# Kernel optimization log

Hardware: AMD Instinct MI355X
Metric: run time of the kernel (lower is better)

Reference implementation:

```python
import jax, jax.numpy as jnp
import numpy as np

C_REG = 50.0  # soft-SVM regularization from __init__ default C=50


def kronecker(A, B):
    # torch: einsum('ab,cd->acbd').view(a*c, b*d)
    return jnp.einsum('ab,cd->acbd', A, B).reshape(
        A.shape[0] * B.shape[0], A.shape[1] * B.shape[1])


def setup_inputs() -> dict:
    key = jax.random.key(0)
    k1, k2, k3, k4 = jax.random.split(key, 4)
    N_c, N_S, N_Q, C, W, H = 16, 25, 15, 3, 32, 32
    D_feat = 640
    S_k = jax.random.normal(k1, (N_c, N_S, C, W, H), dtype=jnp.float32)
    Q_k = jax.random.normal(k2, (N_c, N_Q, C, W, H), dtype=jnp.float32)
    # base_net modeled as Flatten -> Linear(C*W*H, D_feat), no bias
    W_base = jax.random.normal(k3, (C * W * H, D_feat), dtype=jnp.float32) * 0.02
    gamma = jax.random.normal(k4, (1,), dtype=jnp.float32)
    return {"S_k": S_k, "Q_k": Q_k, "W_base": W_base, "gamma": gamma}


def reference(S_k, Q_k, W_base, gamma):
    N_c, N_S = S_k.shape[:2]
    N_Q = Q_k.shape[1]
    # base_net: flatten image dims, project to features
    f_x = S_k.reshape(N_c * N_S, -1) @ W_base  # placeholder
    f_x = Q_k.reshape(N_c * N_Q, -1) @ W_base          # [N_c*N_Q, D]
    K = S_k.reshape(N_c * N_S, -1) @ W_base            # [N_c*N_S, D]
    # kernel matrix + ridge
    aul = K @ K.T + C_REG * jnp.eye(N_c * N_S, dtype=K.dtype)  # [N_c*N_S, N_c*N_S]
    # explicit Kronecker expansion to the full (N_c^2*N_S) system
    Q = kronecker(jnp.eye(N_c, dtype=K.dtype), aul)    # [N_c^2*N_S, N_c^2*N_S]
    p = kronecker(jnp.eye(N_c, dtype=K.dtype),
                  jnp.ones((1, N_S), dtype=K.dtype)).reshape(-1, 1)
    alpha = jnp.linalg.solve(Q, jax.lax.stop_gradient(p))  # p is detached in torch
    alpha = alpha.reshape(N_c, -1)                     # [N_c, N_c*N_S]
    w_k = alpha @ K                                    # [N_c, D]
    logits = -gamma * (f_x @ w_k.T)                    # [N_c*N_Q, N_c]
    return logits
```

## Files before the change

### kernel.cpp

```cpp
#include <hip/hip_runtime.h>
#include <math.h>

#define DIN 3072
#define DF 640
#define MROWS 400
#define QROWS 240
#define NMAT 400
#define PN 416
#define NRHS 16
#define CREG 50.0f
#define PVSTEPS 5
#define CSTEPS 25
#define KSPLIT 4
#define GBLK 13
#define SCOLS 32
#define FPAD 72
#define MTILES 28
#define DPAD 424

typedef __attribute__((ext_vector_type(8))) short bf8v;
typedef __attribute__((ext_vector_type(4))) short s4v;
typedef __attribute__((ext_vector_type(4))) float f32x4;

__device__ __forceinline__ short bf16_rn(float x) {
  unsigned u = __float_as_uint(x);
  u += 0x7FFFu + ((u >> 16) & 1u);
  return (short)(u >> 16);
}
__device__ __forceinline__ void split_sh(float x, short& h, short& l) {
  h = bf16_rn(x);
  float hf = __uint_as_float(((unsigned)(unsigned short)h) << 16);
  l = bf16_rn(x - hf);
}
__device__ __forceinline__ float bf2f(short h) {
  return __uint_as_float(((unsigned)(unsigned short)h) << 16);
}

__global__ __launch_bounds__(256) void gemm_feat_sk(const float* __restrict__ S,
                                                    const float* __restrict__ Qm,
                                                    const float* __restrict__ Wb,
                                                    float* __restrict__ Acc) {
  __shared__ short Ash[64][FPAD];
  __shared__ short Asl[64][FPAD];
  __shared__ short Bsh[64][FPAD];
  __shared__ short Bsl[64][FPAD];
  int tid = threadIdx.x;
  int wave = tid >> 6, lane = tid & 63, l16 = lane & 15, quad = lane >> 4;
  int by = blockIdx.y, bx = blockIdx.x, bz = blockIdx.z;
  int colBase = bx * 64;
  int kbeg = bz * (DIN / KSPLIT), kend = kbeg + (DIN / KSPLIT);
  int kc4 = (tid & 15) * 4;
  float4 ar4[4], br4[4];
  auto load_regs = [&](int kk) {
#pragma unroll
    for (int p = 0; p < 4; ++p) {
      int rowoff = 16 * p;
      const float* srp;
      {
        int ar_ = by * 64 + (tid >> 4) + rowoff;
        srp = (ar_ < MROWS) ? (S + (size_t)ar_ * DIN) : (Qm + (size_t)(ar_ - MROWS) * DIN);
      }
      ar4[p] = *reinterpret_cast<const float4*>(srp + kk + kc4);
      int r = (tid >> 4) + rowoff;
      br4[p] = *reinterpret_cast<const float4*>(Wb + (size_t)(kk + r) * DF + colBase + kc4);
    }
  };
  auto split_write = [&]() {
#pragma unroll
    for (int p = 0; p < 4; ++p) {
      int row = (tid >> 4) + 16 * p;
      s4v hv, lv; short h, l;
      split_sh(ar4[p].x, h, l); hv[0] = h; lv[0] = l;
      split_sh(ar4[p].y, h, l); hv[1] = h; lv[1] = l;
      split_sh(ar4[p].z, h, l); hv[2] = h; lv[2] = l;
      split_sh(ar4[p].w, h, l); hv[3] = h; lv[3] = l;
      *reinterpret_cast<s4v*>(&Ash[row][kc4]) = hv;
      *reinterpret_cast<s4v*>(&Asl[row][kc4]) = lv;
      split_sh(br4[p].x, h, l); Bsh[kc4 + 0][row] = h; Bsl[kc4 + 0][row] = l;
      split_sh(br4[p].y, h, l); Bsh[kc4 + 1][row] = h; Bsl[kc4 + 1][row] = l;
      split_sh(br4[p].z, h, l); Bsh[kc4 + 2][row] = h; Bsl[kc4 + 2][row] = l;
      split_sh(br4[p].w, h, l); Bsh[kc4 + 3][row] = h; Bsl[kc4 + 3][row] = l;
    }
  };
  f32x4 acc[4] = {{0,0,0,0},{0,0,0,0},{0,0,0,0},{0,0,0,0}};
  load_regs(kbeg);
  split_write();
  __syncthreads();
  int k0 = kbeg;
  while (true) {
    int kn = k0 + 64;
    bool more = (kn < kend);
    if (more) load_regs(kn);
#pragma unroll
    for (int kk = 0; kk < 64; kk += 32) {
      int ko = kk + quad * 8;
      bf8v ah = *reinterpret_cast<const bf8v*>(&Ash[wave * 16 + l16][ko]);
      bf8v al = *reinterpret_cast<const bf8v*>(&Asl[wave * 16 + l16][ko]);
#pragma unroll
      for (int t = 0; t < 4; ++t) {
        bf8v bh = *reinterpret_cast<const bf8v*>(&Bsh[t * 16 + l16][ko]);
        bf8v bl = *reinterpret_cast<const bf8v*>(&Bsl[t * 16 + l16][ko]);
        acc[t] = __builtin_amdgcn_mfma_f32_16x16x32_bf16(ah, bh, acc[t], 0, 0, 0);
        acc[t] = __builtin_amdgcn_mfma_f32_16x16x32_bf16(ah, bl, acc[t], 0, 0, 0);
        acc[t] = __builtin_amdgcn_mfma_f32_16x16x32_bf16(al, bh, acc[t], 0, 0, 0);
      }
    }
    if (!more) break;
    __syncthreads();
    split_write();
    __syncthreads();
    k0 = kn;
  }
  float* Ap = Acc + (size_t)bz * 640 * DF;
  int row0 = by * 64 + wave * 16;
#pragma unroll
  for (int t = 0; t < 4; ++t)
#pragma unroll
    for (int r = 0; r < 4; ++r) {
      int row = row0 + quad * 4 + r;
      int col = colBase + t * 16 + l16;
      Ap[(size_t)row * DF + col] = acc[t][r];
    }
}

__global__ __launch_bounds__(256) void feat_reduce(const float* __restrict__ Acc,
                                                   short* __restrict__ Kh,
                                                   short* __restrict__ Kl,
                                                   float* __restrict__ FX,
                                                   float* __restrict__ zbuf,
                                                   float* __restrict__ out) {
  int tid = threadIdx.x;
  if (blockIdx.x == 0) {
    for (int e = tid; e < 16; e += 256) zbuf[e] = 0.f;
  } else if (blockIdx.x == 1) {
    for (int e = tid; e < QROWS * NRHS; e += 256) out[e] = 0.f;
  }
  int idx = blockIdx.x * 256 + tid;
  if (idx >= 640 * DF) return;
  float v = Acc[idx] + Acc[idx + 409600] + Acc[idx + 819200] + Acc[idx + 1228800];
  int row = idx / DF, col = idx - row * DF;
  if (row < MROWS) {
    short h, l; split_sh(v, h, l);
    Kh[(size_t)row * DF + col] = h;
    Kl[(size_t)row * DF + col] = l;
  } else {
    FX[(size_t)(row - MROWS) * DF + col] = v;
  }
}

__global__ __launch_bounds__(256) void gemm_aul(const short* __restrict__ Kh,
                                                const short* __restrict__ Kl,
                                                short* __restrict__ Aph,
                                                short* __restrict__ Apl) {
  int tid = threadIdx.x;
  int wave = tid >> 6, lane = tid & 63;
  int l16 = lane & 15, quad = lane >> 4;
  int row0 = blockIdx.y * 64 + wave * 16;
  int colBase = blockIdx.x * 64;
  bool aValid = (row0 < MROWS);
  const bf8v bzero = {0,0,0,0,0,0,0,0};
  f32x4 acc[4] = {{0,0,0,0},{0,0,0,0},{0,0,0,0},{0,0,0,0}};
  for (int k0 = 0; k0 < DF; k0 += 32) {
    int ka = k0 + quad * 8;
    bf8v ah = bzero, al = bzero;
    if (aValid) {
      size_t ao = (size_t)(row0 + l16) * DF + ka;
      ah = *reinterpret_cast<const bf8v*>(Kh + ao);
      al = *reinterpret_cast<const bf8v*>(Kl + ao);
    }
#pragma unroll
    for (int t = 0; t < 4; ++t) {
      int colt = colBase + t * 16;
      bf8v bh = bzero, bl = bzero;
      if (colt < MROWS) {
        size_t bo = (size_t)(colt + l16) * DF + ka;
        bh = *reinterpret_cast<const bf8v*>(Kh + bo);
        bl = *reinterpret_cast<const bf8v*>(Kl + bo);
      }
      acc[t] = __builtin_amdgcn_mfma_f32_16x16x32_bf16(ah, bh, acc[t], 0, 0, 0);
      acc[t] = __builtin_amdgcn_mfma_f32_16x16x32_bf16(ah, bl, acc[t], 0, 0, 0);
      acc[t] = __builtin_amdgcn_mfma_f32_16x16x32_bf16(al, bh, acc[t], 0, 0, 0);
    }
  }
  if (row0 >= PN) return;
#pragma unroll
  for (int t = 0; t < 4; ++t) {
    int colt = colBase + t * 16;
    if (colt >= PN) continue;
#pragma unroll
    for (int r = 0; r < 4; ++r) {
      int row = row0 + quad * 4 + r;
      int col = colt + l16;
      float v = acc[t][r];
      if (row == col && row < MROWS) v += CREG;
      short h, l; split_sh(v, h, l);
      size_t o = (size_t)row * PN + col;
      Aph[o] = h; Apl[o] = l;
    }
  }
}

__global__ __launch_bounds__(256) void solve_and_m(const short* __restrict__ Aph,
                                                   const short* __restrict__ Apl,
                                                   const float* __restrict__ FX,
                                                   const short* __restrict__ Kh,
                                                   const short* __restrict__ Kl,
                                                   const float* __restrict__ gamma,
                                                   unsigned* __restrict__ D0,
                                                   unsigned* __restrict__ D1,
                                                   float* __restrict__ V0,
                                                   float* __restrict__ V1,
                                                   unsigned* __restrict__ bar,
                                                   unsigned* __restrict__ mflag,
                                                   float* __restrict__ M,
                                                   float* __restrict__ out) {
  int tid = threadIdx.x, b = blockIdx.x;
  int wave = tid >> 6, lane = tid & 63, l16 = lane & 15, quad = lane >> 4;
  const bf8v bzero = {0,0,0,0,0,0,0,0};

  if (b >= GBLK) {
    int mt = b - GBLK;
    int mb = mt / 7, nb = mt - (mt / 7) * 7;
    int q0 = mb * 64 + wave * 16;
    f32x4 acc[4] = {{0,0,0,0},{0,0,0,0},{0,0,0,0},{0,0,0,0}};
    int arow = q0 + l16;
    bool aOk = (arow < QROWS);
    const float* fr = FX + (size_t)(aOk ? arow : 0) * DF;
    for (int k0 = 0; k0 < DF; k0 += 32) {
      int ka = k0 + quad * 8;
      bf8v ah = bzero, al = bzero;
      if (aOk) {
        float4 a0 = *reinterpret_cast<const float4*>(fr + ka);
        float4 a1 = *reinterpret_cast<const float4*>(fr + ka + 4);
        float av[8] = {a0.x, a0.y, a0.z, a0.w, a1.x, a1.y, a1.z, a1.w};
#pragma unroll
        for (int j = 0; j < 8; ++j) { short h, l; split_sh(av[j], h, l); ah[j] = h; al[j] = l; }
      }
#pragma unroll
      for (int t = 0; t < 4; ++t) {
        int n = nb * 64 + t * 16 + l16;
        bf8v bh = bzero, bl = bzero;
        if (n < NMAT) {
          bh = *reinterpret_cast<const bf8v*>(Kh + (size_t)n * DF + ka);
          bl = *reinterpret_cast<const bf8v*>(Kl + (size_t)n * DF + ka);
        }
        acc[t] = __builtin_amdgcn_mfma_f32_16x16x32_bf16(ah, bh, acc[t], 0, 0, 0);
        acc[t] = __builtin_amdgcn_mfma_f32_16x16x32_bf16(ah, bl, acc[t], 0, 0, 0);
        acc[t] = __builtin_amdgcn_mfma_f32_16x16x32_bf16(al, bh, acc[t], 0, 0, 0);
      }
    }
#pragma unroll
    for (int t = 0; t < 4; ++t)
#pragma unroll
      for (int r = 0; r < 4; ++r) {
        int row = q0 + quad * 4 + r;
        int col = nb * 64 + t * 16 + l16;
        if (row < QROWS && col < NMAT)
          __hip_atomic_store(&M[(size_t)row * NMAT + col], acc[t][r],
                             __ATOMIC_RELAXED, __HIP_MEMORY_SCOPE_AGENT);
      }
    __syncthreads();
    if (tid == 0)
      __hip_atomic_fetch_add(mflag, 1u, __ATOMIC_RELEASE, __HIP_MEMORY_SCOPE_AGENT);
    return;
  }

  __shared__ __align__(16) short Abig[2][SCOLS][DPAD];
  __shared__ __align__(16) short dbT[2][NRHS][DPAD];
  __shared__ float yred[4][SCOLS][17];
  __shared__ float vprevL[PN], vcurL[PN];
  __shared__ float XsL[SCOLS][NRHS + 1];
  __shared__ float scal[2];
  __shared__ float rn[4], rd[4];
  int r0 = b * SCOLS;

  for (int e = tid; e < SCOLS * 52; e += 256) {
    int i = e / 52, c = e - i * 52;
    *reinterpret_cast<bf8v*>(&Abig[0][i][c * 8]) =
        *reinterpret_cast<const bf8v*>(Aph + (size_t)(r0 + i) * PN + c * 8);
    *reinterpret_cast<bf8v*>(&Abig[1][i][c * 8]) =
        *reinterpret_cast<const bf8v*>(Apl + (size_t)(r0 + i) * PN + c * 8);
  }
  for (int e = tid; e < NRHS * DPAD; e += 256) (&dbT[0][0][0])[e] = 0;
  for (int e = tid; e < PN; e += 256) {
    float v = (e < NMAT) ? (1.f + 0.125f * (float)(e & 7)) : 0.f;
    vcurL[e] = v;
    dbT[0][0][e] = bf16_rn(v);
  }
  __syncthreads();

  unsigned ph = 0;
  auto gridbar = [&]() {
    __syncthreads();
    ++ph;
    if (tid == 0) {
      unsigned tgt = ph * GBLK;
      __hip_atomic_fetch_add(bar, 1u, __ATOMIC_RELEASE, __HIP_MEMORY_SCOPE_AGENT);
      while (__hip_atomic_load(bar, __ATOMIC_RELAXED, __HIP_MEMORY_SCOPE_AGENT) < tgt)
        __builtin_amdgcn_s_sleep(2);
    }
    __syncthreads();
  };

  auto matvec = [&](bool lo) {
    f32x4 acc0 = {0, 0, 0, 0}, acc1 = {0, 0, 0, 0};
    for (int kt = wave; kt < 13; kt += 4) {
      int ko = kt * 32 + quad * 8;
      bf8v bh = *reinterpret_cast<const bf8v*>(&dbT[0][l16][ko]);
      bf8v ah0 = *reinterpret_cast<const bf8v*>(&Abig[0][l16][ko]);
      bf8v ah1 = *reinterpret_cast<const bf8v*>(&Abig[0][16 + l16][ko]);
      acc0 = __builtin_amdgcn_mfma_f32_16x16x32_bf16(ah0, bh, acc0, 0, 0, 0);
      acc1 = __builtin_amdgcn_mfma_f32_16x16x32_bf16(ah1, bh, acc1, 0, 0, 0);
      if (lo) {
        bf8v bl = *reinterpret_cast<const bf8v*>(&dbT[1][l16][ko]);
        bf8v al0 = *reinterpret_cast<const bf8v*>(&Abig[1][l16][ko]);
        bf8v al1 = *reinterpret_cast<const bf8v*>(&Abig[1][16 + l16][ko]);
        acc0 = __builtin_amdgcn_mfma_f32_16x16x32_bf16(ah0, bl, acc0, 0, 0, 0);
        acc0 = __builtin_amdgcn_mfma_f32_16x16x32_bf16(al0, bh, acc0, 0, 0, 0);
        acc1 = __builtin_amdgcn_mfma_f32_16x16x32_bf16(ah1, bl, acc1, 0, 0, 0);
        acc1 = __builtin_amdgcn_mfma_f32_16x16x32_bf16(al1, bh, acc1, 0, 0, 0);
      }
    }
#pragma unroll
    for (int r_ = 0; r_ < 4; ++r_) {
      yred[wave][quad * 4 + r_][l16] = acc0[r_];
      yred[wave][16 + quad * 4 + r_][l16] = acc1[r_];
    }
  };

  for (int s = 0; s < PVSTEPS; ++s) {
    matvec(false);
    __syncthreads();
    if (tid < SCOLS) {
      float y = yred[0][tid][0] + yred[1][tid][0] + yred[2][tid][0] + yred[3][tid][0];
      float* Vb = (s & 1) ? V1 : V0;
      __hip_atomic_store(&Vb[r0 + tid], y, __ATOMIC_RELAXED, __HIP_MEMORY_SCOPE_AGENT);
    }
    gridbar();
    const float* Vb = (s & 1) ? V1 : V0;
    if (s == PVSTEPS - 1)
      for (int e = tid; e < PN; e += 256) vprevL[e] = vcurL[e];
    float g0 = __hip_atomic_load(&Vb[tid], __ATOMIC_RELAXED, __HIP_MEMORY_SCOPE_AGENT);
    float g1 = (tid < PN - 256)
        ? __hip_atomic_load(&Vb[tid + 256], __ATOMIC_RELAXED, __HIP_MEMORY_SCOPE_AGENT)
        : 0.f;
    {
      float v = g0 * (1.f / 4096.f);
      vcurL[tid] = v;
      dbT[0][0][tid] = bf16_rn(v);
    }
    if (tid < PN - 256) {
      float v = g1 * (1.f / 4096.f);
      vcurL[tid + 256] = v;
      dbT[0][0][tid + 256] = bf16_rn(v);
    }
    __syncthreads();
  }

  {
    float n = 0.f, dd = 0.f;
    for (int e = tid; e < PN; e += 256) {
      n += vprevL[e] * vcurL[e];
      dd += vprevL[e] * vprevL[e];
    }
#pragma unroll
    for (int o = 32; o; o >>= 1) {
      n += __shfl_down(n, o);
      dd += __shfl_down(dd, o);
    }
    if (lane == 0) { rn[wave] = n; rd[wave] = dd; }
    __syncthreads();
    if (tid == 0) {
      float N = rn[0] + rn[1] + rn[2] + rn[3];
      float D = rd[0] + rd[1] + rd[2] + rd[3];
      float rqv = 4096.f * N / D;
      float bb = 1.3f * rqv;
      if (!(bb > 800.f)) bb = 12000.f;
      if (bb > 100000.f) bb = 100000.f;
      scal[0] = 0.5f * (bb + CREG);
      scal[1] = 0.5f * (bb - CREG);
    }
    __syncthreads();
  }
  float theta = scal[0], delta = scal[1];
  float sigma = theta / delta, rho = 1.f / sigma;

  float xr[2], rr[2], dr[2];
#pragma unroll
  for (int m = 0; m < 2; ++m) {
    int rl = (tid >> 4) + 16 * m, c = tid & 15, gi = r0 + rl;
    float pc = (gi < NMAT && (gi / 25) == c) ? 1.f : 0.f;
    xr[m] = 0.f; rr[m] = pc; dr[m] = pc / theta;
    short h, l; split_sh(dr[m], h, l);
    __hip_atomic_store(&D0[(size_t)gi * NRHS + c],
                       ((unsigned)(unsigned short)h << 16) | (unsigned)(unsigned short)l,
                       __ATOMIC_RELAXED, __HIP_MEMORY_SCOPE_AGENT);
  }
  gridbar();
  {
    unsigned gw[26];
#pragma unroll
    for (int j = 0; j < 26; ++j)
      gw[j] = __hip_atomic_load(&D0[tid + 256 * j], __ATOMIC_RELAXED, __HIP_MEMORY_SCOPE_AGENT);
#pragma unroll
    for (int j = 0; j < 26; ++j) {
      int e = tid + 256 * j, row = e >> 4, c = e & 15;
      dbT[0][c][row] = (short)(gw[j] >> 16);
      dbT[1][c][row] = (short)gw[j];
    }
  }
  __syncthreads();

  for (int k = 0; k < CSTEPS - 1; ++k) {
    matvec(true);
    __syncthreads();
    float rho1 = 1.f / (2.f * sigma - rho);
    float s1 = rho1 * rho, s2 = 2.f * rho1 / delta;
    rho = rho1;
    unsigned* Db = (k & 1) ? D0 : D1;
#pragma unroll
    for (int m = 0; m < 2; ++m) {
      int rl = (tid >> 4) + 16 * m, c = tid & 15, gi = r0 + rl;
      float mv = yred[0][rl][c] + yred[1][rl][c] + yred[2][rl][c] + yred[3][rl][c];
      xr[m] += dr[m];
      rr[m] -= mv;
      float dn = s1 * dr[m] + s2 * rr[m];
      dr[m] = dn;
      if (k < CSTEPS - 2) {
        short h, l; split_sh(dn, h, l);
        __hip_atomic_store(&Db[(size_t)gi * NRHS + c],
                           ((unsigned)(unsigned short)h << 16) | (unsigned)(unsigned short)l,
                           __ATOMIC_RELAXED, __HIP_MEMORY_SCOPE_AGENT);
      }
    }
    if (k < CSTEPS - 2) {
      gridbar();
      unsigned gw[26];
#pragma unroll
      for (int j = 0; j < 26; ++j)
        gw[j] = __hip_atomic_load(&Db[tid + 256 * j], __ATOMIC_RELAXED, __HIP_MEMORY_SCOPE_AGENT);
#pragma unroll
      for (int j = 0; j < 26; ++j) {
        int e = tid + 256 * j, row = e >> 4, c = e & 15;
        dbT[0][c][row] = (short)(gw[j] >> 16);
        dbT[1][c][row] = (short)gw[j];
      }
    }
    __syncthreads();
  }

#pragma unroll
  for (int m = 0; m < 2; ++m) {
    int rl = (tid >> 4) + 16 * m, c = tid & 15;
    XsL[rl][c] = xr[m] + dr[m];
  }
  __syncthreads();
  if (tid == 0) {
    while (__hip_atomic_load(mflag, __ATOMIC_RELAXED, __HIP_MEMORY_SCOPE_AGENT) < MTILES)
      __builtin_amdgcn_s_sleep(2);
  }
  __syncthreads();
  float* Msl = reinterpret_cast<float*>(&Abig[0][0][0]);
  {
    float gm[30];
#pragma unroll
    for (int j = 0; j < 30; ++j) {
      int e = tid + 256 * j;
      int q = e >> 5, i = e & 31;
      gm[j] = (r0 + i < NMAT)
                  ? __hip_atomic_load(&M[(size_t)q * NMAT + r0 + i],
                                      __ATOMIC_RELAXED, __HIP_MEMORY_SCOPE_AGENT)
                  : 0.f;
    }
#pragma unroll
    for (int j = 0; j < 30; ++j) Msl[tid + 256 * j] = gm[j];
  }
  __syncthreads();
  float g = -gamma[0];
  int c = tid & 15;
  for (int q = tid >> 4; q < QROWS; q += 16) {
    float s = 0.f;
#pragma unroll
    for (int i = 0; i < SCOLS; ++i) s += Msl[q * SCOLS + i] * XsL[i][c];
    atomicAdd(&out[q * NRHS + c], g * s);
  }
}

extern "C" void kernel_launch(void* const* d_in, const int* in_sizes, int n_in,
                              void* d_out, int out_size, void* d_ws, size_t ws_size,
                              hipStream_t stream) {
  const float* S = (const float*)d_in[0];
  const float* Qm = (const float*)d_in[1];
  const float* Wb = (const float*)d_in[2];
  const float* gamma = (const float*)d_in[3];
  float* out = (float*)d_out;
  char* base = (char*)d_ws;
  short* Kh   = (short*)(base);
  short* Kl   = (short*)(base + 512000);
  float* FX   = (float*)(base + 1024000);
  short* Aph  = (short*)(base + 1638400);
  short* Apl  = (short*)(base + 1984512);
  float* Mm   = (float*)(base + 2330624);
  unsigned* bar = (unsigned*)(base + 2740224);
  unsigned* mflag = (unsigned*)(base + 2740240);
  float* zbuf = (float*)(base + 2740224);
  unsigned* D0 = (unsigned*)(base + 2740288);
  unsigned* D1 = (unsigned*)(base + 2766912);
  float* V0   = (float*)(base + 2793536);
  float* V1   = (float*)(base + 2795200);
  float* Acc  = (float*)(base + 2796864);

  gemm_feat_sk<<<dim3(10, 10, KSPLIT), 256, 0, stream>>>(S, Qm, Wb, Acc);
  feat_reduce<<<1600, 256, 0, stream>>>(Acc, Kh, Kl, FX, zbuf, out);
  gemm_aul<<<dim3(7, 7), 256, 0, stream>>>(Kh, Kl, Aph, Apl);
  solve_and_m<<<GBLK + MTILES, 256, 0, stream>>>(Aph, Apl, FX, Kh, Kl, gamma,
                                                 D0, D1, V0, V1, bar, mflag,
                                                 Mm, out);
}
```

Measured before the change: 216.0 us.

## Fuse kernel-matrix GEMM into solver and replace grid barrier with per-block flags

Removes the separate gemm_aul launch. Each solver block now computes its own 32-row slab of K·Kᵀ+C·I directly into shared memory with split-bf16 MFMAs. The single atomic grid barrier is replaced by per-block progress flags, so each wave waits only for the producer blocks whose slice it consumes and can start its partial matvec as soon as those arrive. This removes one kernel launch, the global round-trip of the matrix, and full-grid synchronisation. In exchange, the 13 solver blocks do redundant reads of K and more serial GEMM work, and a zeroed flags region is assumed across overlapping workspace offsets.

```diff
diff --git a/kernel.cpp b/kernel.cpp
--- a/kernel.cpp
+++ b/kernel.cpp
@@ -32,9 +32,6 @@
   float hf = __uint_as_float(((unsigned)(unsigned short)h) << 16);
   l = bf16_rn(x - hf);
 }
-__device__ __forceinline__ float bf2f(short h) {
-  return __uint_as_float(((unsigned)(unsigned short)h) << 16);
-}
 
 __global__ __launch_bounds__(256) void gemm_feat_sk(const float* __restrict__ S,
                                                     const float* __restrict__ Qm,
@@ -148,61 +145,7 @@
   }
 }
 
-__global__ __launch_bounds__(256) void gemm_aul(const short* __restrict__ Kh,
-                                                const short* __restrict__ Kl,
-                                                short* __restrict__ Aph,
-                                                short* __restrict__ Apl) {
-  int tid = threadIdx.x;
-  int wave = tid >> 6, lane = tid & 63;
-  int l16 = lane & 15, quad = lane >> 4;
-  int row0 = blockIdx.y * 64 + wave * 16;
-  int colBase = blockIdx.x * 64;
-  bool aValid = (row0 < MROWS);
-  const bf8v bzero = {0,0,0,0,0,0,0,0};
-  f32x4 acc[4] = {{0,0,0,0},{0,0,0,0},{0,0,0,0},{0,0,0,0}};
-  for (int k0 = 0; k0 < DF; k0 += 32) {
-    int ka = k0 + quad * 8;
-    bf8v ah = bzero, al = bzero;
-    if (aValid) {
-      size_t ao = (size_t)(row0 + l16) * DF + ka;
-      ah = *reinterpret_cast<const bf8v*>(Kh + ao);
-      al = *reinterpret_cast<const bf8v*>(Kl + ao);
-    }
-#pragma unroll
-    for (int t = 0; t < 4; ++t) {
-      int colt = colBase + t * 16;
-      bf8v bh = bzero, bl = bzero;
-      if (colt < MROWS) {
-        size_t bo = (size_t)(colt + l16) * DF + ka;
-        bh = *reinterpret_cast<const bf8v*>(Kh + bo);
-        bl = *reinterpret_cast<const bf8v*>(Kl + bo);
-      }
-      acc[t] = __builtin_amdgcn_mfma_f32_16x16x32_bf16(ah, bh, acc[t], 0, 0, 0);
-      acc[t] = __builtin_amdgcn_mfma_f32_16x16x32_bf16(ah, bl, acc[t], 0, 0, 0);
-      acc[t] = __builtin_amdgcn_mfma_f32_16x16x32_bf16(al, bh, acc[t], 0, 0, 0);
-    }
-  }
-  if (row0 >= PN) return;
-#pragma unroll
-  for (int t = 0; t < 4; ++t) {
-    int colt = colBase + t * 16;
-    if (colt >= PN) continue;
-#pragma unroll
-    for (int r = 0; r < 4; ++r) {
-      int row = row0 + quad * 4 + r;
-      int col = colt + l16;
-      float v = acc[t][r];
-      if (row == col && row < MROWS) v += CREG;
-      short h, l; split_sh(v, h, l);
-      size_t o = (size_t)row * PN + col;
-      Aph[o] = h; Apl[o] = l;
-    }
-  }
-}
-
-__global__ __launch_bounds__(256) void solve_and_m(const short* __restrict__ Aph,
-                                                   const short* __restrict__ Apl,
-                                                   const float* __restrict__ FX,
+__global__ __launch_bounds__(256) void solve_and_m(const float* __restrict__ FX,
                                                    const short* __restrict__ Kh,
                                                    const short* __restrict__ Kl,
                                                    const float* __restrict__ gamma,
@@ -210,7 +153,7 @@
                                                    unsigned* __restrict__ D1,
                                                    float* __restrict__ V0,
                                                    float* __restrict__ V1,
-                                                   unsigned* __restrict__ bar,
+                                                   unsigned* __restrict__ flags,
                                                    unsigned* __restrict__ mflag,
                                                    float* __restrict__ M,
                                                    float* __restrict__ out) {
@@ -274,14 +217,69 @@
   __shared__ float rn[4], rd[4];
   int r0 = b * SCOLS;
 
-  for (int e = tid; e < SCOLS * 52; e += 256) {
-    int i = e / 52, c = e - i * 52;
-    *reinterpret_cast<bf8v*>(&Abig[0][i][c * 8]) =
-        *reinterpret_cast<const bf8v*>(Aph + (size_t)(r0 + i) * PN + c * 8);
-    *reinterpret_cast<bf8v*>(&Abig[1][i][c * 8]) =
-        *reinterpret_cast<const bf8v*>(Apl + (size_t)(r0 + i) * PN + c * 8);
-  }
-  for (int e = tid; e < NRHS * DPAD; e += 256) (&dbT[0][0][0])[e] = 0;
+  for (int e = tid; e < SCOLS * DPAD; e += 256) {
+    *reinterpret_cast<unsigned*>(&(&Abig[0][0][0])[e * 2]) = 0u;
+    *reinterpret_cast<unsigned*>(&(&Abig[1][0][0])[e * 2]) = 0u;
+  }
+  for (int e = tid; e < NRHS * DPAD; e += 256) {
+    (&dbT[0][0][0])[e] = 0; (&dbT[1][0][0])[e] = 0;
+  }
+  __syncthreads();
+
+  {
+    bool rg1ok = (r0 + 16) < MROWS;
+    f32x4 pacc[2][7];
+#pragma unroll
+    for (int j = 0; j < 7; ++j) { pacc[0][j] = {0,0,0,0}; pacc[1][j] = {0,0,0,0}; }
+    const short* kh0 = Kh + (size_t)(r0 + l16) * DF;
+    const short* kl0 = Kl + (size_t)(r0 + l16) * DF;
+    const short* kh1 = Kh + (size_t)(rg1ok ? (r0 + 16 + l16) : 0) * DF;
+    const short* kl1 = Kl + (size_t)(rg1ok ? (r0 + 16 + l16) : 0) * DF;
+    for (int k0 = 0; k0 < DF; k0 += 32) {
+      int ka = k0 + quad * 8;
+      bf8v ah0 = *reinterpret_cast<const bf8v*>(kh0 + ka);
+      bf8v al0 = *reinterpret_cast<const bf8v*>(kl0 + ka);
+      bf8v ah1 = *reinterpret_cast<const bf8v*>(kh1 + ka);
+      bf8v al1 = *reinterpret_cast<const bf8v*>(kl1 + ka);
+#pragma unroll
+      for (int j = 0; j < 7; ++j) {
+        int cg = wave + 4 * j;
+        if (cg < 25) {
+          const short* bhp = Kh + (size_t)(cg * 16 + l16) * DF + ka;
+          const short* blp = Kl + (size_t)(cg * 16 + l16) * DF + ka;
+          bf8v bh = *reinterpret_cast<const bf8v*>(bhp);
+          bf8v bl = *reinterpret_cast<const bf8v*>(blp);
+          pacc[0][j] = __builtin_amdgcn_mfma_f32_16x16x32_bf16(ah0, bh, pacc[0][j], 0, 0, 0);
+          pacc[0][j] = __builtin_amdgcn_mfma_f32_16x16x32_bf16(ah0, bl, pacc[0][j], 0, 0, 0);
+          pacc[0][j] = __builtin_amdgcn_mfma_f32_16x16x32_bf16(al0, bh, pacc[0][j], 0, 0, 0);
+          pacc[1][j] = __builtin_amdgcn_mfma_f32_16x16x32_bf16(ah1, bh, pacc[1][j], 0, 0, 0);
+          pacc[1][j] = __builtin_amdgcn_mfma_f32_16x16x32_bf16(ah1, bl, pacc[1][j], 0, 0, 0);
+          pacc[1][j] = __builtin_amdgcn_mfma_f32_16x16x32_bf16(al1, bh, pacc[1][j], 0, 0, 0);
+        }
+      }
+    }
+#pragma unroll
+    for (int j = 0; j < 7; ++j) {
+      int cg = wave + 4 * j;
+      if (cg < 25) {
+#pragma unroll
+        for (int rg = 0; rg < 2; ++rg) {
+          if (rg == 1 && !rg1ok) continue;
+#pragma unroll
+          for (int r = 0; r < 4; ++r) {
+            int lrow = rg * 16 + quad * 4 + r;
+            int col = cg * 16 + l16;
+            float v = pacc[rg][j][r];
+            if (r0 + lrow == col) v += CREG;
+            short h, l; split_sh(v, h, l);
+            Abig[0][lrow][col] = h;
+            Abig[1][lrow][col] = l;
+          }
+        }
+      }
+    }
+  }
+
   for (int e = tid; e < PN; e += 256) {
     float v = (e < NMAT) ? (1.f + 0.125f * (float)(e & 7)) : 0.f;
     vcurL[e] = v;
@@ -289,36 +287,30 @@
   }
   __syncthreads();
 
-  unsigned ph = 0;
-  auto gridbar = [&]() {
-    __syncthreads();
-    ++ph;
-    if (tid == 0) {
-      unsigned tgt = ph * GBLK;
-      __hip_atomic_fetch_add(bar, 1u, __ATOMIC_RELEASE, __HIP_MEMORY_SCOPE_AGENT);
-      while (__hip_atomic_load(bar, __ATOMIC_RELAXED, __HIP_MEMORY_SCOPE_AGENT) < tgt)
-        __builtin_amdgcn_s_sleep(2);
-    }
-    __syncthreads();
-  };
-
-  auto matvec = [&](bool lo) {
-    f32x4 acc0 = {0, 0, 0, 0}, acc1 = {0, 0, 0, 0};
-    for (int kt = wave; kt < 13; kt += 4) {
-      int ko = kt * 32 + quad * 8;
-      bf8v bh = *reinterpret_cast<const bf8v*>(&dbT[0][l16][ko]);
-      bf8v ah0 = *reinterpret_cast<const bf8v*>(&Abig[0][l16][ko]);
-      bf8v ah1 = *reinterpret_cast<const bf8v*>(&Abig[0][16 + l16][ko]);
-      acc0 = __builtin_amdgcn_mfma_f32_16x16x32_bf16(ah0, bh, acc0, 0, 0, 0);
-      acc1 = __builtin_amdgcn_mfma_f32_16x16x32_bf16(ah1, bh, acc1, 0, 0, 0);
-      if (lo) {
-        bf8v bl = *reinterpret_cast<const bf8v*>(&dbT[1][l16][ko]);
-        bf8v al0 = *reinterpret_cast<const bf8v*>(&Abig[1][l16][ko]);
-        bf8v al1 = *reinterpret_cast<const bf8v*>(&Abig[1][16 + l16][ko]);
-        acc0 = __builtin_amdgcn_mfma_f32_16x16x32_bf16(ah0, bl, acc0, 0, 0, 0);
-        acc0 = __builtin_amdgcn_mfma_f32_16x16x32_bf16(al0, bh, acc0, 0, 0, 0);
-        acc1 = __builtin_amdgcn_mfma_f32_16x16x32_bf16(ah1, bl, acc1, 0, 0, 0);
-        acc1 = __builtin_amdgcn_mfma_f32_16x16x32_bf16(al1, bh, acc1, 0, 0, 0);
+  for (int s = 0; s < PVSTEPS; ++s) {
+    f32x4 acc0 = {0,0,0,0}, acc1 = {0,0,0,0};
+    const float* Vprev = ((s - 1) & 1) ? V1 : V0;
+#pragma unroll
+    for (int t = 0; t < 4; ++t) {
+      int j = wave + 4 * t;
+      if (j < GBLK) {
+        if (s > 0) {
+          while (__hip_atomic_load(&flags[j], __ATOMIC_RELAXED, __HIP_MEMORY_SCOPE_AGENT) < (unsigned)s)
+            __builtin_amdgcn_s_sleep(1);
+          if (lane < 32) {
+            float y = __hip_atomic_load((float*)&Vprev[32 * j + lane],
+                                        __ATOMIC_RELAXED, __HIP_MEMORY_SCOPE_AGENT);
+            float v = y * (1.f / 4096.f);
+            vcurL[32 * j + lane] = v;
+            dbT[0][0][32 * j + lane] = bf16_rn(v);
+          }
+        }
+        int ko = j * 32 + quad * 8;
+        bf8v bh = *reinterpret_cast<const bf8v*>(&dbT[0][l16][ko]);
+        bf8v ah0 = *reinterpret_cast<const bf8v*>(&Abig[0][l16][ko]);
+        bf8v ah1 = *reinterpret_cast<const bf8v*>(&Abig[0][16 + l16][ko]);
+        acc0 = __builtin_amdgcn_mfma_f32_16x16x32_bf16(ah0, bh, acc0, 0, 0, 0);
+        acc1 = __builtin_amdgcn_mfma_f32_16x16x32_bf16(ah1, bh, acc1, 0, 0, 0);
       }
     }
 #pragma unroll
@@ -326,37 +318,36 @@
       yred[wave][quad * 4 + r_][l16] = acc0[r_];
       yred[wave][16 + quad * 4 + r_][l16] = acc1[r_];
     }
-  };
-
-  for (int s = 0; s < PVSTEPS; ++s) {
-    matvec(false);
     __syncthreads();
     if (tid < SCOLS) {
       float y = yred[0][tid][0] + yred[1][tid][0] + yred[2][tid][0] + yred[3][tid][0];
       float* Vb = (s & 1) ? V1 : V0;
       __hip_atomic_store(&Vb[r0 + tid], y, __ATOMIC_RELAXED, __HIP_MEMORY_SCOPE_AGENT);
     }
-    gridbar();
-    const float* Vb = (s & 1) ? V1 : V0;
-    if (s == PVSTEPS - 1)
-      for (int e = tid; e < PN; e += 256) vprevL[e] = vcurL[e];
-    float g0 = __hip_atomic_load(&Vb[tid], __ATOMIC_RELAXED, __HIP_MEMORY_SCOPE_AGENT);
-    float g1 = (tid < PN - 256)
-        ? __hip_atomic_load(&Vb[tid + 256], __ATOMIC_RELAXED, __HIP_MEMORY_SCOPE_AGENT)
-        : 0.f;
-    {
-      float v = g0 * (1.f / 4096.f);
-      vcurL[tid] = v;
-      dbT[0][0][tid] = bf16_rn(v);
-    }
-    if (tid < PN - 256) {
-      float v = g1 * (1.f / 4096.f);
-      vcurL[tid + 256] = v;
-      dbT[0][0][tid + 256] = bf16_rn(v);
-    }
-    __syncthreads();
-  }
-
+    __syncthreads();
+    if (tid == 0)
+      __hip_atomic_store(&flags[b], (unsigned)(s + 1), __ATOMIC_RELEASE, __HIP_MEMORY_SCOPE_AGENT);
+  }
+
+  for (int e = tid; e < PN; e += 256) vprevL[e] = vcurL[e];
+  __syncthreads();
+  {
+    const float* Vb = ((PVSTEPS - 1) & 1) ? V1 : V0;
+#pragma unroll
+    for (int t = 0; t < 4; ++t) {
+      int j = wave + 4 * t;
+      if (j < GBLK) {
+        while (__hip_atomic_load(&flags[j], __ATOMIC_RELAXED, __HIP_MEMORY_SCOPE_AGENT) < (unsigned)PVSTEPS)
+          __builtin_amdgcn_s_sleep(1);
+        if (lane < 32) {
+          float y = __hip_atomic_load((float*)&Vb[32 * j + lane],
+                                      __ATOMIC_RELAXED, __HIP_MEMORY_SCOPE_AGENT);
+          vcurL[32 * j + lane] = y * (1.f / 4096.f);
+        }
+      }
+    }
+  }
+  __syncthreads();
   {
     float n = 0.f, dd = 0.f;
     for (int e = tid; e < PN; e += 256) {
@@ -396,28 +387,75 @@
                        ((unsigned)(unsigned short)h << 16) | (unsigned)(unsigned short)l,
                        __ATOMIC_RELAXED, __HIP_MEMORY_SCOPE_AGENT);
   }
-  gridbar();
-  {
-    unsigned gw[26];
-#pragma unroll
-    for (int j = 0; j < 26; ++j)
-      gw[j] = __hip_atomic_load(&D0[tid + 256 * j], __ATOMIC_RELAXED, __HIP_MEMORY_SCOPE_AGENT);
-#pragma unroll
-    for (int j = 0; j < 26; ++j) {
-      int e = tid + 256 * j, row = e >> 4, c = e & 15;
-      dbT[0][c][row] = (short)(gw[j] >> 16);
-      dbT[1][c][row] = (short)gw[j];
-    }
-  }
-  __syncthreads();
+  __syncthreads();
+  if (tid == 0)
+    __hip_atomic_store(&flags[b], (unsigned)(PVSTEPS + 1), __ATOMIC_RELEASE, __HIP_MEMORY_SCOPE_AGENT);
 
   for (int k = 0; k < CSTEPS - 1; ++k) {
-    matvec(true);
+    unsigned tgt = (unsigned)(PVSTEPS + 1 + k);
+    const unsigned* Db = (k & 1) ? D1 : D0;
+#pragma unroll
+    for (int t = 0; t < 4; ++t) {
+      int j = wave + 4 * t;
+      if (j < GBLK) {
+        while (__hip_atomic_load((unsigned*)&flags[j], __ATOMIC_RELAXED, __HIP_MEMORY_SCOPE_AGENT) < tgt)
+          __builtin_amdgcn_s_sleep(1);
+      }
+    }
+    unsigned gw[4][8];
+#pragma unroll
+    for (int t = 0; t < 4; ++t) {
+      int j = wave + 4 * t;
+      if (j < GBLK) {
+        const unsigned* src = Db + 512 * j;
+#pragma unroll
+        for (int q = 0; q < 8; ++q)
+          gw[t][q] = __hip_atomic_load((unsigned*)&src[lane + 64 * q],
+                                       __ATOMIC_RELAXED, __HIP_MEMORY_SCOPE_AGENT);
+      }
+    }
+#pragma unroll
+    for (int t = 0; t < 4; ++t) {
+      int j = wave + 4 * t;
+      if (j < GBLK) {
+#pragma unroll
+        for (int q = 0; q < 8; ++q) {
+          int e = lane + 64 * q, row = 32 * j + (e >> 4), c = e & 15;
+          dbT[0][c][row] = (short)(gw[t][q] >> 16);
+          dbT[1][c][row] = (short)gw[t][q];
+        }
+      }
+    }
+    f32x4 acc0 = {0,0,0,0}, acc1 = {0,0,0,0};
+#pragma unroll
+    for (int t = 0; t < 4; ++t) {
+      int kt = wave + 4 * t;
+      if (kt < GBLK) {
+        int ko = kt * 32 + quad * 8;
+        bf8v bh = *reinterpret_cast<const bf8v*>(&dbT[0][l16][ko]);
+        bf8v bl = *reinterpret_cast<const bf8v*>(&dbT[1][l16][ko]);
+        bf8v ah0 = *reinterpret_cast<const bf8v*>(&Abig[0][l16][ko]);
+        bf8v al0 = *reinterpret_cast<const bf8v*>(&Abig[1][l16][ko]);
+        bf8v ah1 = *reinterpret_cast<const bf8v*>(&Abig[0][16 + l16][ko]);
+        bf8v al1 = *reinterpret_cast<const bf8v*>(&Abig[1][16 + l16][ko]);
+        acc0 = __builtin_amdgcn_mfma_f32_16x16x32_bf16(ah0, bh, acc0, 0, 0, 0);
+        acc0 = __builtin_amdgcn_mfma_f32_16x16x32_bf16(ah0, bl, acc0, 0, 0, 0);
+        acc0 = __builtin_amdgcn_mfma_f32_16x16x32_bf16(al0, bh, acc0, 0, 0, 0);
+        acc1 = __builtin_amdgcn_mfma_f32_16x16x32_bf16(ah1, bh, acc1, 0, 0, 0);
+        acc1 = __builtin_amdgcn_mfma_f32_16x16x32_bf16(ah1, bl, acc1, 0, 0, 0);
+        acc1 = __builtin_amdgcn_mfma_f32_16x16x32_bf16(al1, bh, acc1, 0, 0, 0);
+      }
+    }
+#pragma unroll
+    for (int r_ = 0; r_ < 4; ++r_) {
+      yred[wave][quad * 4 + r_][l16] = acc0[r_];
+      yred[wave][16 + quad * 4 + r_][l16] = acc1[r_];
+    }
     __syncthreads();
     float rho1 = 1.f / (2.f * sigma - rho);
     float s1 = rho1 * rho, s2 = 2.f * rho1 / delta;
     rho = rho1;
-    unsigned* Db = (k & 1) ? D0 : D1;
+    unsigned* Dn = (k & 1) ? D0 : D1;
 #pragma unroll
     for (int m = 0; m < 2; ++m) {
       int rl = (tid >> 4) + 16 * m, c = tid & 15, gi = r0 + rl;
@@ -428,25 +466,14 @@
       dr[m] = dn;
       if (k < CSTEPS - 2) {
         short h, l; split_sh(dn, h, l);
-        __hip_atomic_store(&Db[(size_t)gi * NRHS + c],
+        __hip_atomic_store(&Dn[(size_t)gi * NRHS + c],
                            ((unsigned)(unsigned short)h << 16) | (unsigned)(unsigned short)l,
                            __ATOMIC_RELAXED, __HIP_MEMORY_SCOPE_AGENT);
       }
     }
-    if (k < CSTEPS - 2) {
-      gridbar();
-      unsigned gw[26];
-#pragma unroll
-      for (int j = 0; j < 26; ++j)
-        gw[j] = __hip_atomic_load(&Db[tid + 256 * j], __ATOMIC_RELAXED, __HIP_MEMORY_SCOPE_AGENT);
-#pragma unroll
-      for (int j = 0; j < 26; ++j) {
-        int e = tid + 256 * j, row = e >> 4, c = e & 15;
-        dbT[0][c][row] = (short)(gw[j] >> 16);
-        dbT[1][c][row] = (short)gw[j];
-      }
-    }
-    __syncthreads();
+    __syncthreads();
+    if (k < CSTEPS - 2 && tid == 0)
+      __hip_atomic_store(&flags[b], tgt + 1, __ATOMIC_RELEASE, __HIP_MEMORY_SCOPE_AGENT);
   }
 
 #pragma unroll
@@ -498,11 +525,9 @@
   short* Kh   = (short*)(base);
   short* Kl   = (short*)(base + 512000);
   float* FX   = (float*)(base + 1024000);
-  short* Aph  = (short*)(base + 1638400);
-  short* Apl  = (short*)(base + 1984512);
   float* Mm   = (float*)(base + 2330624);
-  unsigned* bar = (unsigned*)(base + 2740224);
-  unsigned* mflag = (unsigned*)(base + 2740240);
+  unsigned* flags = (unsigned*)(base + 2740224);
+  unsigned* mflag = (unsigned*)(base + 2740224 + 52);
   float* zbuf = (float*)(base + 2740224);
   unsigned* D0 = (unsigned*)(base + 2740288);
   unsigned* D1 = (unsigned*)(base + 2766912);
@@ -512,8 +537,7 @@
 
   gemm_feat_sk<<<dim3(10, 10, KSPLIT), 256, 0, stream>>>(S, Qm, Wb, Acc);
   feat_reduce<<<1600, 256, 0, stream>>>(Acc, Kh, Kl, FX, zbuf, out);
-  gemm_aul<<<dim3(7, 7), 256, 0, stream>>>(Kh, Kl, Aph, Apl);
-  solve_and_m<<<GBLK + MTILES, 256, 0, stream>>>(Aph, Apl, FX, Kh, Kl, gamma,
-                                                 D0, D1, V0, V1, bar, mflag,
+  solve_and_m<<<GBLK + MTILES, 256, 0, stream>>>(FX, Kh, Kl, gamma,
+                                                 D0, D1, V0, V1, flags, mflag,
                                                  Mm, out);
 }
```

Result: slower. 254.6 us (+17.9%).

## Fuse kernel-matrix GEMM into solver kernel with per-row-block readiness flags

Applied to the files above, without the earlier changes.

Removes the separate gemm_aul launch and computes the regularized kernel matrix inside solve_and_m using 49 extra blocks. The results are stored as packed hi/lo bf16 words via atomic stores, and per-row-block counters signal readiness. Solver blocks spin on the flag for their row block before loading their slice. This saves one kernel launch and its boundary gap, and lets the M GEMM and A GEMM overlap. It relies on all blocks being co-resident to avoid deadlock and adds element-wise atomic loads when filling LDS.

```diff
diff --git a/kernel.cpp b/kernel.cpp
--- a/kernel.cpp
+++ b/kernel.cpp
@@ -16,6 +16,7 @@
 #define SCOLS 32
 #define FPAD 72
 #define MTILES 28
+#define ATILES 49
 #define DPAD 424
 
 typedef __attribute__((ext_vector_type(8))) short bf8v;
@@ -31,9 +32,6 @@
   h = bf16_rn(x);
   float hf = __uint_as_float(((unsigned)(unsigned short)h) << 16);
   l = bf16_rn(x - hf);
-}
-__device__ __forceinline__ float bf2f(short h) {
-  return __uint_as_float(((unsigned)(unsigned short)h) << 16);
 }
 
 __global__ __launch_bounds__(256) void gemm_feat_sk(const float* __restrict__ S,
@@ -128,10 +126,12 @@
                                                    short* __restrict__ Kl,
                                                    float* __restrict__ FX,
                                                    float* __restrict__ zbuf,
+                                                   unsigned* __restrict__ aflags,
                                                    float* __restrict__ out) {
   int tid = threadIdx.x;
   if (blockIdx.x == 0) {
-    for (int e = tid; e < 16; e += 256) zbuf[e] = 0.f;
+    if (tid < 16) zbuf[tid] = 0.f;
+    if (tid < 8) aflags[tid] = 0u;
   } else if (blockIdx.x == 1) {
     for (int e = tid; e < QROWS * NRHS; e += 256) out[e] = 0.f;
   }
@@ -148,75 +148,76 @@
   }
 }
 
-__global__ __launch_bounds__(256) void gemm_aul(const short* __restrict__ Kh,
-                                                const short* __restrict__ Kl,
-                                                short* __restrict__ Aph,
-                                                short* __restrict__ Apl) {
-  int tid = threadIdx.x;
-  int wave = tid >> 6, lane = tid & 63;
-  int l16 = lane & 15, quad = lane >> 4;
-  int row0 = blockIdx.y * 64 + wave * 16;
-  int colBase = blockIdx.x * 64;
-  bool aValid = (row0 < MROWS);
-  const bf8v bzero = {0,0,0,0,0,0,0,0};
-  f32x4 acc[4] = {{0,0,0,0},{0,0,0,0},{0,0,0,0},{0,0,0,0}};
-  for (int k0 = 0; k0 < DF; k0 += 32) {
-    int ka = k0 + quad * 8;
-    bf8v ah = bzero, al = bzero;
-    if (aValid) {
-      size_t ao = (size_t)(row0 + l16) * DF + ka;
-      ah = *reinterpret_cast<const bf8v*>(Kh + ao);
-      al = *reinterpret_cast<const bf8v*>(Kl + ao);
-    }
-#pragma unroll
-    for (int t = 0; t < 4; ++t) {
-      int colt = colBase + t * 16;
-      bf8v bh = bzero, bl = bzero;
-      if (colt < MROWS) {
-        size_t bo = (size_t)(colt + l16) * DF + ka;
-        bh = *reinterpret_cast<const bf8v*>(Kh + bo);
-        bl = *reinterpret_cast<const bf8v*>(Kl + bo);
-      }
-      acc[t] = __builtin_amdgcn_mfma_f32_16x16x32_bf16(ah, bh, acc[t], 0, 0, 0);
-      acc[t] = __builtin_amdgcn_mfma_f32_16x16x32_bf16(ah, bl, acc[t], 0, 0, 0);
-      acc[t] = __builtin_amdgcn_mfma_f32_16x16x32_bf16(al, bh, acc[t], 0, 0, 0);
-    }
-  }
-  if (row0 >= PN) return;
-#pragma unroll
-  for (int t = 0; t < 4; ++t) {
-    int colt = colBase + t * 16;
-    if (colt >= PN) continue;
-#pragma unroll
-    for (int r = 0; r < 4; ++r) {
-      int row = row0 + quad * 4 + r;
-      int col = colt + l16;
-      float v = acc[t][r];
-      if (row == col && row < MROWS) v += CREG;
-      short h, l; split_sh(v, h, l);
-      size_t o = (size_t)row * PN + col;
-      Aph[o] = h; Apl[o] = l;
-    }
-  }
-}
-
-__global__ __launch_bounds__(256) void solve_and_m(const short* __restrict__ Aph,
-                                                   const short* __restrict__ Apl,
-                                                   const float* __restrict__ FX,
+__global__ __launch_bounds__(256) void solve_and_m(const float* __restrict__ FX,
                                                    const short* __restrict__ Kh,
                                                    const short* __restrict__ Kl,
                                                    const float* __restrict__ gamma,
+                                                   unsigned* __restrict__ Apk,
                                                    unsigned* __restrict__ D0,
                                                    unsigned* __restrict__ D1,
                                                    float* __restrict__ V0,
                                                    float* __restrict__ V1,
                                                    unsigned* __restrict__ bar,
                                                    unsigned* __restrict__ mflag,
+                                                   unsigned* __restrict__ aflags,
                                                    float* __restrict__ M,
                                                    float* __restrict__ out) {
   int tid = threadIdx.x, b = blockIdx.x;
   int wave = tid >> 6, lane = tid & 63, l16 = lane & 15, quad = lane >> 4;
   const bf8v bzero = {0,0,0,0,0,0,0,0};
+
+  if (b >= GBLK + MTILES) {
+    int ab = b - GBLK - MTILES;
+    int bx_ = ab % 7, by_ = ab / 7;
+    int row0 = by_ * 64 + wave * 16;
+    int colBase = bx_ * 64;
+    bool aValid = (row0 < MROWS);
+    f32x4 acc[4] = {{0,0,0,0},{0,0,0,0},{0,0,0,0},{0,0,0,0}};
+    for (int k0 = 0; k0 < DF; k0 += 32) {
+      int ka = k0 + quad * 8;
+      bf8v ah = bzero, al = bzero;
+      if (aValid) {
+        size_t ao = (size_t)(row0 + l16) * DF + ka;
+        ah = *reinterpret_cast<const bf8v*>(Kh + ao);
+        al = *reinterpret_cast<const bf8v*>(Kl + ao);
+      }
+#pragma unroll
+      for (int t = 0; t < 4; ++t) {
+        int colt = colBase + t * 16;
+        bf8v bh = bzero, bl = bzero;
+        if (colt < MROWS) {
+          size_t bo = (size_t)(colt + l16) * DF + ka;
+          bh = *reinterpret_cast<const bf8v*>(Kh + bo);
+          bl = *reinterpret_cast<const bf8v*>(Kl + bo);
+        }
+        acc[t] = __builtin_amdgcn_mfma_f32_16x16x32_bf16(ah, bh, acc[t], 0, 0, 0);
+        acc[t] = __builtin_amdgcn_mfma_f32_16x16x32_bf16(ah, bl, acc[t], 0, 0, 0);
+        acc[t] = __builtin_amdgcn_mfma_f32_16x16x32_bf16(al, bh, acc[t], 0, 0, 0);
+      }
+    }
+    if (row0 < PN) {
+#pragma unroll
+      for (int t = 0; t < 4; ++t) {
+        int colt = colBase + t * 16;
+        if (colt >= PN) continue;
+#pragma unroll
+        for (int r = 0; r < 4; ++r) {
+          int row = row0 + quad * 4 + r;
+          int col = colt + l16;
+          float v = acc[t][r];
+          if (row == col && row < MROWS) v += CREG;
+          short h, l; split_sh(v, h, l);
+          __hip_atomic_store(&Apk[(size_t)row * PN + col],
+                             ((unsigned)(unsigned short)h << 16) | (unsigned)(unsigned short)l,
+                             __ATOMIC_RELAXED, __HIP_MEMORY_SCOPE_AGENT);
+        }
+      }
+    }
+    __syncthreads();
+    if (tid == 0)
+      __hip_atomic_fetch_add(&aflags[by_], 1u, __ATOMIC_RELEASE, __HIP_MEMORY_SCOPE_AGENT);
+    return;
+  }
 
   if (b >= GBLK) {
     int mt = b - GBLK;
@@ -274,18 +275,26 @@
   __shared__ float rn[4], rd[4];
   int r0 = b * SCOLS;
 
-  for (int e = tid; e < SCOLS * 52; e += 256) {
-    int i = e / 52, c = e - i * 52;
-    *reinterpret_cast<bf8v*>(&Abig[0][i][c * 8]) =
-        *reinterpret_cast<const bf8v*>(Aph + (size_t)(r0 + i) * PN + c * 8);
-    *reinterpret_cast<bf8v*>(&Abig[1][i][c * 8]) =
-        *reinterpret_cast<const bf8v*>(Apl + (size_t)(r0 + i) * PN + c * 8);
-  }
-  for (int e = tid; e < NRHS * DPAD; e += 256) (&dbT[0][0][0])[e] = 0;
+  for (int e = tid; e < NRHS * DPAD; e += 256) {
+    (&dbT[0][0][0])[e] = 0; (&dbT[1][0][0])[e] = 0;
+  }
   for (int e = tid; e < PN; e += 256) {
     float v = (e < NMAT) ? (1.f + 0.125f * (float)(e & 7)) : 0.f;
     vcurL[e] = v;
     dbT[0][0][e] = bf16_rn(v);
+  }
+
+  if (tid == 0) {
+    while (__hip_atomic_load(&aflags[b >> 1], __ATOMIC_RELAXED, __HIP_MEMORY_SCOPE_AGENT) < 7u)
+      __builtin_amdgcn_s_sleep(2);
+  }
+  __syncthreads();
+  for (int e = tid; e < SCOLS * PN; e += 256) {
+    int i = e / PN, c = e - i * PN;
+    unsigned w = __hip_atomic_load(&Apk[(size_t)(r0 + i) * PN + c],
+                                   __ATOMIC_RELAXED, __HIP_MEMORY_SCOPE_AGENT);
+    Abig[0][i][c] = (short)(w >> 16);
+    Abig[1][i][c] = (short)w;
   }
   __syncthreads();
 
@@ -340,9 +349,9 @@
     const float* Vb = (s & 1) ? V1 : V0;
     if (s == PVSTEPS - 1)
       for (int e = tid; e < PN; e += 256) vprevL[e] = vcurL[e];
-    float g0 = __hip_atomic_load(&Vb[tid], __ATOMIC_RELAXED, __HIP_MEMORY_SCOPE_AGENT);
+    float g0 = __hip_atomic_load((float*)&Vb[tid], __ATOMIC_RELAXED, __HIP_MEMORY_SCOPE_AGENT);
     float g1 = (tid < PN - 256)
-        ? __hip_atomic_load(&Vb[tid + 256], __ATOMIC_RELAXED, __HIP_MEMORY_SCOPE_AGENT)
+        ? __hip_atomic_load((float*)&Vb[tid + 256], __ATOMIC_RELAXED, __HIP_MEMORY_SCOPE_AGENT)
         : 0.f;
     {
       float v = g0 * (1.f / 4096.f);
@@ -498,11 +507,11 @@
   short* Kh   = (short*)(base);
   short* Kl   = (short*)(base + 512000);
   float* FX   = (float*)(base + 1024000);
-  short* Aph  = (short*)(base + 1638400);
-  short* Apl  = (short*)(base + 1984512);
+  unsigned* Apk = (unsigned*)(base + 1638400);
   float* Mm   = (float*)(base + 2330624);
+  unsigned* aflags = (unsigned*)(base + 2714624);
   unsigned* bar = (unsigned*)(base + 2740224);
-  unsigned* mflag = (unsigned*)(base + 2740240);
+  unsigned* mflag = (unsigned*)(base + 2740224 + 52);
   float* zbuf = (float*)(base + 2740224);
   unsigned* D0 = (unsigned*)(base + 2740288);
   unsigned* D1 = (unsigned*)(base + 2766912);
@@ -511,9 +520,8 @@
   float* Acc  = (float*)(base + 2796864);
 
   gemm_feat_sk<<<dim3(10, 10, KSPLIT), 256, 0, stream>>>(S, Qm, Wb, Acc);
-  feat_reduce<<<1600, 256, 0, stream>>>(Acc, Kh, Kl, FX, zbuf, out);
-  gemm_aul<<<dim3(7, 7), 256, 0, stream>>>(Kh, Kl, Aph, Apl);
-  solve_and_m<<<GBLK + MTILES, 256, 0, stream>>>(Aph, Apl, FX, Kh, Kl, gamma,
-                                                 D0, D1, V0, V1, bar, mflag,
-                                                 Mm, out);
+  feat_reduce<<<1600, 256, 0, stream>>>(Acc, Kh, Kl, FX, zbuf, aflags, out);
+  solve_and_m<<<GBLK + MTILES + ATILES, 256, 0, stream>>>(FX, Kh, Kl, gamma, Apk,
+                                                          D0, D1, V0, V1, bar,
+                                                          mflag, aflags, Mm, out);
 }
```

New measurement: 226.6 us. 1.05x slower.
